# Performance work log

Measured on AMD Instinct MI355X. Metric: run time of the kernel, lower is better.

The kernel has to match this reference:

```python
import jax, jax.numpy as jnp
import numpy as np

ALPHA = 6.0
BETA = 1.8
D = 256
P = 4096


def setup_inputs() -> dict:
    key = jax.random.key(0)
    k1, k2, k3 = jax.random.split(key, 3)
    pts = jax.random.normal(k1, (1, 16384, 3), dtype=jnp.float32)
    # strict_standard_normal is a shuffled Gaussian quantile grid; a standard
    # normal draw is statistically equivalent for a correctness baseline.
    A = jax.random.normal(k2, (3, D), dtype=jnp.float32) * ALPHA
    B = jax.random.normal(k3, (3, P), dtype=jnp.float32) * BETA
    return {"pts": pts, "A": A, "B": B}


def reference(pts, A, B):
    d = A.shape[-1]
    sqrt_d = jnp.asarray(d, jnp.float32) ** 0.5
    pA = pts @ A            # (b, n, d)
    pB = pts @ B            # (b, n, p)
    eA = jnp.concatenate([jnp.cos(pA), jnp.sin(pA)], axis=-1)  # (b, n, 2d)
    eB = jnp.concatenate([jnp.cos(pB), jnp.sin(pB)], axis=-1)  # (b, n, 2p)
    # linear-attention-style chain: eB @ (eB^T @ eA)
    T = jnp.einsum('bnp,bnd->bpd', eB, eA)   # (b, 2p, 2d)
    G = jnp.einsum('bnp,bpd->bnd', eB, T)    # (b, n, 2d)
    Gc = jax.lax.complex(G[..., :d], G[..., d:]) / jax.lax.complex(eA[..., :d], eA[..., d:])
    Gc = Gc / jnp.linalg.norm(Gc, axis=-1, keepdims=True) * sqrt_d
    return Gc
```

## Files before the change

### kernel.cpp

```cpp
#include <hip/hip_runtime.h>

#define NPTS 16384
#define DH 256
#define PH 4096
#define D2 512

typedef _Float16 f16;
typedef _Float16 f16x4 __attribute__((ext_vector_type(4)));
typedef _Float16 f16x8 __attribute__((ext_vector_type(8)));
typedef float f32x4 __attribute__((ext_vector_type(4)));

__device__ f16   g_eAtS[(size_t)D2 * NPTS];
__device__ f16   g_Tt[4][D2][2*PH];
__device__ f16   g_TsS[(size_t)D2 * 2*PH];
__device__ float g_G[2][NPTS][D2];

__device__ __forceinline__ void gload16(const void* g, void* l) {
    __builtin_amdgcn_global_load_lds((const __attribute__((address_space(1))) void*)g,
                                     (__attribute__((address_space(3))) void*)l, 16, 0, 0);
}

__device__ __forceinline__ void fsincos(float x, float* s, float* c) {
    *s = __sinf(x); *c = __cosf(x);
}

__global__ __launch_bounds__(256) void ker_pre(const float* __restrict__ pts,
                                               const float* __restrict__ A) {
    const int dd = blockIdx.x;
    const int t  = threadIdx.x;
    const float a0 = A[dd], a1 = A[DH + dd], a2 = A[2*DH + dd];
    f16* rowc = &g_eAtS[(size_t)dd*NPTS + t*64];
    f16* rows = &g_eAtS[(size_t)(DH + dd)*NPTS + t*64];
    const int sx = dd & 7;
    #pragma unroll
    for (int s = 0; s < 8; ++s) {
        const int nb = t*64 + 8*(s ^ sx);
        f16x8 vc, vs;
        #pragma unroll
        for (int i = 0; i < 8; ++i) {
            const float* pr = pts + (size_t)(nb + i)*3;
            float sn, cs_; fsincos(pr[0]*a0 + pr[1]*a1 + pr[2]*a2, &sn, &cs_);
            vc[i] = (f16)cs_; vs[i] = (f16)sn;
        }
        *(f16x8*)(rowc + 8*s) = vc;
        *(f16x8*)(rows + 8*s) = vs;
    }
}

__global__ __launch_bounds__(512) void ker_T(const float* __restrict__ pts,
                                             const float* __restrict__ B) {
    const int q0 = blockIdx.x * 64;
    const int d0 = blockIdx.y * 256;
    const int ks = blockIdx.z;
    const int t  = threadIdx.x;
    const int lane = t & 63, wid = t >> 6;
    const int wm = wid >> 2, wn = wid & 3;
    const int l7 = lane & 7;

    __shared__ f16 Al[128][64];
    __shared__ f16 Bl[256][64];

    f32x4 acc[4][4];
    #pragma unroll
    for (int a = 0; a < 4; ++a)
        #pragma unroll
        for (int bq = 0; bq < 4; ++bq) acc[a][bq] = (f32x4){0.f,0.f,0.f,0.f};

    const int qq  = t >> 3;
    const int nn0 = (t & 7) * 8;
    const int wsl = ((t & 7) ^ (qq & 7)) * 8;
    const float b0 = B[q0+qq], b1 = B[PH+q0+qq], b2 = B[2*PH+q0+qq];
    const size_t bsrc0 = (size_t)(d0 + 32*wid + (lane >> 3))*NPTS + 8*l7;
    const int mrow = wm*64 + (lane & 15);
    const int ncol = wn*64 + (lane & 15);

    f16x8 vcR, vsR;

#define TSB(nb_)                                                               \
    _Pragma("unroll")                                                          \
    for (int i = 0; i < 4; ++i)                                                \
        gload16(&g_eAtS[0] + bsrc0 + (size_t)(8*i)*NPTS + (size_t)(nb_),       \
                &Bl[32*wid + 8*i][0])

#define TCOMP(nb_) do {                                                        \
    const float* pb = pts + (size_t)((nb_) + nn0)*3;                           \
    const float4 F0 = *(const float4*)(pb);                                    \
    const float4 F1 = *(const float4*)(pb + 4);                                \
    const float4 F2 = *(const float4*)(pb + 8);                                \
    const float4 F3 = *(const float4*)(pb + 12);                               \
    const float4 F4 = *(const float4*)(pb + 16);                               \
    const float4 F5 = *(const float4*)(pb + 20);                               \
    const float xx[8] = {F0.x, F0.w, F1.z, F2.y, F3.x, F3.w, F4.z, F5.y};      \
    const float yy[8] = {F0.y, F1.x, F1.w, F2.z, F3.y, F4.x, F4.w, F5.z};      \
    const float zz[8] = {F0.z, F1.y, F2.x, F2.w, F3.z, F4.y, F5.x, F5.w};      \
    _Pragma("unroll")                                                          \
    for (int u = 0; u < 8; ++u) {                                              \
        float sn, cc; fsincos(xx[u]*b0 + yy[u]*b1 + zz[u]*b2, &sn, &cc);       \
        vcR[u] = (f16)cc; vsR[u] = (f16)sn;                                    \
    }                                                                          \
} while (0)

    TCOMP(ks*4096);

    for (int c = 0; c < 64; ++c) {
        const int nb = ks*4096 + c*64;
        TSB(nb);
        *(f16x8*)&Al[qq][wsl]      = vcR;
        *(f16x8*)&Al[64 + qq][wsl] = vsR;
        __syncthreads();
        f16x8 af[2][4], bf[2][4];
        #pragma unroll
        for (int kk = 0; kk < 2; ++kk) {
            #pragma unroll
            for (int mf = 0; mf < 4; ++mf)
                af[kk][mf] = *(const f16x8*)&Al[mrow + mf*16][(((lane >> 4) + 4*kk) ^ l7)*8];
            #pragma unroll
            for (int nf = 0; nf < 4; ++nf)
                bf[kk][nf] = *(const f16x8*)&Bl[ncol + nf*16][(((lane >> 4) + 4*kk) ^ l7)*8];
        }
        if (c < 63) TCOMP(nb + 64);
        #pragma unroll
        for (int kk = 0; kk < 2; ++kk)
            #pragma unroll
            for (int mf = 0; mf < 4; ++mf)
                #pragma unroll
                for (int nf = 0; nf < 4; ++nf)
                    acc[mf][nf] = __builtin_amdgcn_mfma_f32_16x16x32_f16(
                        af[kk][mf], bf[kk][nf], acc[mf][nf], 0, 0, 0);
        asm volatile("" : "+v"(vcR), "+v"(vsR));
        __syncthreads();
    }
#undef TSB
#undef TCOMP

    #pragma unroll
    for (int mf = 0; mf < 4; ++mf) {
        const int qrow = q0 + mf*16 + (lane >> 4)*4;
        #pragma unroll
        for (int nf = 0; nf < 4; ++nf) {
            const int d = d0 + wn*64 + nf*16 + (lane & 15);
            f16x4 v;
            #pragma unroll
            for (int j = 0; j < 4; ++j) v[j] = (f16)acc[mf][nf][j];
            *(f16x4*)&g_Tt[ks][d][(size_t)wm*PH + qrow] = v;
        }
    }
}

__global__ __launch_bounds__(256) void ker_tsum() {
    const int u  = blockIdx.x*256 + threadIdx.x;
    const int d  = u >> 10;
    const int jj = u & 1023;
    const int c = jj >> 3, s = jj & 7;
    const int klb = 64*c + 8*(s ^ (d & 7));
    const int q0_ = klb >> 1;
    float oc[4] = {0,0,0,0}, os[4] = {0,0,0,0};
    #pragma unroll
    for (int z = 0; z < 4; ++z) {
        const f16x4 a  = *(const f16x4*)&g_Tt[z][d][q0_];
        const f16x4 bs = *(const f16x4*)&g_Tt[z][d][PH + q0_];
        #pragma unroll
        for (int j = 0; j < 4; ++j) { oc[j] += (float)a[j]; os[j] += (float)bs[j]; }
    }
    f16x8 v;
    #pragma unroll
    for (int j = 0; j < 4; ++j) { v[2*j] = (f16)oc[j]; v[2*j+1] = (f16)os[j]; }
    *(f16x8*)&g_TsS[(size_t)d*(2*PH) + 64*c + 8*s] = v;
}

__global__ __launch_bounds__(512) void ker_G(const float* __restrict__ pts,
                                             const float* __restrict__ B) {
    const int n0 = blockIdx.x * 128;
    const int d0 = blockIdx.y * 256;
    const int ks = blockIdx.z;
    const int t  = threadIdx.x;
    const int lane = t & 63, wid = t >> 6;
    const int wm = wid >> 2, wn = wid & 3;
    const int l7 = lane & 7;

    __shared__ f16 Al[128][64];
    __shared__ f16 Bl[256][64];

    f32x4 acc[4][4];
    #pragma unroll
    for (int a = 0; a < 4; ++a)
        #pragma unroll
        for (int bq = 0; bq < 4; ++bq) acc[a][bq] = (f32x4){0.f,0.f,0.f,0.f};

    const int nn   = t >> 2;
    const int qch8 = (t & 3) * 8;
    const int sl0  = 2*(t & 3);
    const int sx   = nn & 7;
    const float px = pts[(size_t)(n0+nn)*3];
    const float py = pts[(size_t)(n0+nn)*3 + 1];
    const float pz = pts[(size_t)(n0+nn)*3 + 2];
    const size_t bsrc0 = (size_t)(d0 + 32*wid + (lane >> 3))*(2*PH) + 8*l7;
    const int mrow = wm*64 + (lane & 15);
    const int ncol = wn*64 + (lane & 15);

    f16x8 v0R, v1R;

#define GSB(ikb_)                                                              \
    _Pragma("unroll")                                                          \
    for (int i = 0; i < 4; ++i)                                                \
        gload16(&g_TsS[0] + bsrc0 + (size_t)(8*i)*(2*PH) + (size_t)(ikb_),     \
                &Bl[32*wid + 8*i][0])

#define GCOMP(ikb_) do {                                                       \
    const int qg = ((ikb_) >> 1) + qch8;                                       \
    const float4 X0 = *(const float4*)&B[qg];                                  \
    const float4 X1 = *(const float4*)&B[qg + 4];                              \
    const float4 Y0 = *(const float4*)&B[PH + qg];                             \
    const float4 Y1 = *(const float4*)&B[PH + qg + 4];                         \
    const float4 Z0 = *(const float4*)&B[2*PH + qg];                           \
    const float4 Z1 = *(const float4*)&B[2*PH + qg + 4];                       \
    const float bx[8] = {X0.x,X0.y,X0.z,X0.w, X1.x,X1.y,X1.z,X1.w};            \
    const float by[8] = {Y0.x,Y0.y,Y0.z,Y0.w, Y1.x,Y1.y,Y1.z,Y1.w};            \
    const float bz[8] = {Z0.x,Z0.y,Z0.z,Z0.w, Z1.x,Z1.y,Z1.z,Z1.w};            \
    _Pragma("unroll")                                                          \
    for (int u = 0; u < 8; ++u) {                                              \
        float sn, cc; fsincos(px*bx[u] + py*by[u] + pz*bz[u], &sn, &cc);       \
        if (u < 4) { v0R[2*u]     = (f16)cc; v0R[2*u+1]     = (f16)sn; }       \
        else       { v1R[2*(u-4)] = (f16)cc; v1R[2*(u-4)+1] = (f16)sn; }       \
    }                                                                          \
} while (0)

    GCOMP(ks*4096);

    for (int c = 0; c < 64; ++c) {
        const int ikb = ks*4096 + c*64;
        GSB(ikb);
        *(f16x8*)&Al[nn][((sl0    ) ^ sx)*8] = v0R;
        *(f16x8*)&Al[nn][((sl0 + 1) ^ sx)*8] = v1R;
        __syncthreads();
        f16x8 af[2][4], bf[2][4];
        #pragma unroll
        for (int kk = 0; kk < 2; ++kk) {
            #pragma unroll
            for (int mf = 0; mf < 4; ++mf)
                af[kk][mf] = *(const f16x8*)&Al[mrow + mf*16][(((lane >> 4) + 4*kk) ^ l7)*8];
            #pragma unroll
            for (int nf = 0; nf < 4; ++nf)
                bf[kk][nf] = *(const f16x8*)&Bl[ncol + nf*16][(((lane >> 4) + 4*kk) ^ l7)*8];
        }
        if (c < 63) GCOMP(ikb + 64);
        #pragma unroll
        for (int kk = 0; kk < 2; ++kk)
            #pragma unroll
            for (int mf = 0; mf < 4; ++mf)
                #pragma unroll
                for (int nf = 0; nf < 4; ++nf)
                    acc[mf][nf] = __builtin_amdgcn_mfma_f32_16x16x32_f16(
                        af[kk][mf], bf[kk][nf], acc[mf][nf], 0, 0, 0);
        asm volatile("" : "+v"(v0R), "+v"(v1R));
        __syncthreads();
    }
#undef GSB
#undef GCOMP

    #pragma unroll
    for (int mf = 0; mf < 4; ++mf) {
        const int nbase = n0 + wm*64 + mf*16 + (lane >> 4)*4;
        #pragma unroll
        for (int nf = 0; nf < 4; ++nf) {
            const int d = d0 + wn*64 + nf*16 + (lane & 15);
            #pragma unroll
            for (int j = 0; j < 4; ++j)
                g_G[ks][nbase + j][d] = acc[mf][nf][j];
        }
    }
}

__global__ __launch_bounds__(256) void ker_fin(const float* __restrict__ pts,
                                               const float* __restrict__ A,
                                               float* __restrict__ out) {
    const int n = blockIdx.x;
    const int k = threadIdx.x;
    const float p0 = pts[(size_t)n*3], p1 = pts[(size_t)n*3+1], p2 = pts[(size_t)n*3+2];
    const float alp = p0*A[k] + p1*A[DH + k] + p2*A[2*DH + k];
    float sa, ca; fsincos(alp, &sa, &ca);
    const float Gr = g_G[0][n][k]      + g_G[1][n][k];
    const float Gi = g_G[0][n][DH + k] + g_G[1][n][DH + k];
    const float Re = Gr*ca + Gi*sa;
    float nr = Gr*Gr + Gi*Gi;
    #pragma unroll
    for (int off = 32; off > 0; off >>= 1) nr += __shfl_down(nr, off, 64);
    __shared__ float wsum[4];
    if ((k & 63) == 0) wsum[k >> 6] = nr;
    __syncthreads();
    const float total = wsum[0] + wsum[1] + wsum[2] + wsum[3];
    const float scale = 16.0f * rsqrtf(total);
    out[(size_t)n*DH + k] = Re * scale;
}

extern "C" void kernel_launch(void* const* d_in, const int* in_sizes, int n_in,
                              void* d_out, int out_size, void* d_ws, size_t ws_size,
                              hipStream_t stream) {
    const float* pts = (const float*)d_in[0];
    const float* A   = (const float*)d_in[1];
    const float* B   = (const float*)d_in[2];
    float* out = (float*)d_out;
    (void)d_ws; (void)ws_size; (void)out_size;

    ker_pre <<<256, 256, 0, stream>>>(pts, A);
    ker_T   <<<dim3(64, 2, 4), 512, 0, stream>>>(pts, B);
    ker_tsum<<<2048, 256, 0, stream>>>();
    ker_G   <<<dim3(128, 2, 2), 512, 0, stream>>>(pts, B);
    ker_fin <<<16384, 256, 0, stream>>>(pts, A, out);
}
```

Before: 363.1 us.

## Pipeline GEMM k-loop with triple-buffered async B loads and double-buffered A tile

Both GEMM kernels (T and G) move from a 64-wide k step with one shared buffer and two full syncthreads per step to a 32-wide k step. The B tile is triple-buffered and fetched asynchronously two steps ahead with direct global-to-LDS loads. The A tile is double-buffered and written by the on-the-fly sin/cos computation, with a single barrier per step guarded by explicit vmcnt/lgkmcnt waits. Global intermediate layouts lose their XOR swizzle, and LDS bank conflicts are instead avoided with a padded A row stride and a lane-dependent rotation on B reads. The goal is to overlap memory latency with MFMA work and halve barriers per k element, at the cost of twice as many loop iterations and hand-tuned wait counts that could be fragile.

```diff
diff --git a/kernel.cpp b/kernel.cpp
--- a/kernel.cpp
+++ b/kernel.cpp
@@ -4,15 +4,16 @@
 #define DH 256
 #define PH 4096
 #define D2 512
+#define LDA 40
 
 typedef _Float16 f16;
 typedef _Float16 f16x4 __attribute__((ext_vector_type(4)));
 typedef _Float16 f16x8 __attribute__((ext_vector_type(8)));
 typedef float f32x4 __attribute__((ext_vector_type(4)));
 
-__device__ f16   g_eAtS[(size_t)D2 * NPTS];
+__device__ f16   g_eAt[D2][NPTS];
 __device__ f16   g_Tt[4][D2][2*PH];
-__device__ f16   g_TsS[(size_t)D2 * 2*PH];
+__device__ f16   g_Ts[D2][2*PH];
 __device__ float g_G[2][NPTS][D2];
 
 __device__ __forceinline__ void gload16(const void* g, void* l) {
@@ -29,12 +30,11 @@
     const int dd = blockIdx.x;
     const int t  = threadIdx.x;
     const float a0 = A[dd], a1 = A[DH + dd], a2 = A[2*DH + dd];
-    f16* rowc = &g_eAtS[(size_t)dd*NPTS + t*64];
-    f16* rows = &g_eAtS[(size_t)(DH + dd)*NPTS + t*64];
-    const int sx = dd & 7;
+    f16* rowc = &g_eAt[dd][t*64];
+    f16* rows = &g_eAt[DH + dd][t*64];
     #pragma unroll
     for (int s = 0; s < 8; ++s) {
-        const int nb = t*64 + 8*(s ^ sx);
+        const int nb = t*64 + 8*s;
         f16x8 vc, vs;
         #pragma unroll
         for (int i = 0; i < 8; ++i) {
@@ -55,10 +55,9 @@
     const int t  = threadIdx.x;
     const int lane = t & 63, wid = t >> 6;
     const int wm = wid >> 2, wn = wid & 3;
-    const int l7 = lane & 7;
-
-    __shared__ f16 Al[128][64];
-    __shared__ f16 Bl[256][64];
+
+    __shared__ f16 Al[2][128][LDA];
+    __shared__ f16 Bl[3][256][32];
 
     f32x4 acc[4][4];
     #pragma unroll
@@ -67,71 +66,75 @@
         for (int bq = 0; bq < 4; ++bq) acc[a][bq] = (f32x4){0.f,0.f,0.f,0.f};
 
     const int qq  = t >> 3;
-    const int nn0 = (t & 7) * 8;
-    const int wsl = ((t & 7) ^ (qq & 7)) * 8;
+    const int nn0 = (t & 7) * 4;
     const float b0 = B[q0+qq], b1 = B[PH+q0+qq], b2 = B[2*PH+q0+qq];
-    const size_t bsrc0 = (size_t)(d0 + 32*wid + (lane >> 3))*NPTS + 8*l7;
+    const int phiL = (((lane >> 2) & 3) + (lane >> 4)) & 3;
+    const size_t bsrc0 = (size_t)(d0 + 32*wid + (lane >> 2))*NPTS
+                       + 8 * ((lane & 3) ^ phiL);
     const int mrow = wm*64 + (lane & 15);
     const int ncol = wn*64 + (lane & 15);
-
-    f16x8 vcR, vsR;
-
-#define TSB(nb_)                                                               \
+    const int akof = (lane >> 4) * 8;
+    const int phib = ((lane & 3) + ((lane >> 2) & 3)) & 3;
+    const int bkof = ((lane >> 4) ^ phib) * 8;
+
+#define TSB(rg, nb_) do {                                                      \
+    gload16(&g_eAt[0][0] + bsrc0 + (size_t)(nb_),              &Bl[rg][32*wid][0]);      \
+    gload16(&g_eAt[0][0] + bsrc0 + (size_t)16*NPTS + (size_t)(nb_), &Bl[rg][32*wid+16][0]); \
+} while (0)
+
+#define TRIG(ab, nb_) do {                                                     \
+    const float* pb = pts + (size_t)((nb_) + nn0)*3;                           \
+    const float4 P0 = *(const float4*)(pb);                                    \
+    const float4 P1 = *(const float4*)(pb + 4);                                \
+    const float4 P2 = *(const float4*)(pb + 8);                                \
+    const float xx[4] = {P0.x, P0.w, P1.z, P2.y};                              \
+    const float yy[4] = {P0.y, P1.x, P1.w, P2.z};                              \
+    const float zz[4] = {P0.z, P1.y, P2.x, P2.w};                              \
+    f16x4 vc, vs;                                                              \
     _Pragma("unroll")                                                          \
-    for (int i = 0; i < 4; ++i)                                                \
-        gload16(&g_eAtS[0] + bsrc0 + (size_t)(8*i)*NPTS + (size_t)(nb_),       \
-                &Bl[32*wid + 8*i][0])
-
-#define TCOMP(nb_) do {                                                        \
-    const float* pb = pts + (size_t)((nb_) + nn0)*3;                           \
-    const float4 F0 = *(const float4*)(pb);                                    \
-    const float4 F1 = *(const float4*)(pb + 4);                                \
-    const float4 F2 = *(const float4*)(pb + 8);                                \
-    const float4 F3 = *(const float4*)(pb + 12);                               \
-    const float4 F4 = *(const float4*)(pb + 16);                               \
-    const float4 F5 = *(const float4*)(pb + 20);                               \
-    const float xx[8] = {F0.x, F0.w, F1.z, F2.y, F3.x, F3.w, F4.z, F5.y};      \
-    const float yy[8] = {F0.y, F1.x, F1.w, F2.z, F3.y, F4.x, F4.w, F5.z};      \
-    const float zz[8] = {F0.z, F1.y, F2.x, F2.w, F3.z, F4.y, F5.x, F5.w};      \
-    _Pragma("unroll")                                                          \
-    for (int u = 0; u < 8; ++u) {                                              \
+    for (int u = 0; u < 4; ++u) {                                              \
         float sn, cc; fsincos(xx[u]*b0 + yy[u]*b1 + zz[u]*b2, &sn, &cc);       \
-        vcR[u] = (f16)cc; vsR[u] = (f16)sn;                                    \
+        vc[u] = (f16)cc; vs[u] = (f16)sn;                                      \
     }                                                                          \
+    *(f16x4*)&Al[ab][qq][nn0]      = vc;                                       \
+    *(f16x4*)&Al[ab][64 + qq][nn0] = vs;                                       \
 } while (0)
 
-    TCOMP(ks*4096);
-
-    for (int c = 0; c < 64; ++c) {
-        const int nb = ks*4096 + c*64;
-        TSB(nb);
-        *(f16x8*)&Al[qq][wsl]      = vcR;
-        *(f16x8*)&Al[64 + qq][wsl] = vsR;
-        __syncthreads();
-        f16x8 af[2][4], bf[2][4];
-        #pragma unroll
-        for (int kk = 0; kk < 2; ++kk) {
-            #pragma unroll
-            for (int mf = 0; mf < 4; ++mf)
-                af[kk][mf] = *(const f16x8*)&Al[mrow + mf*16][(((lane >> 4) + 4*kk) ^ l7)*8];
+    const int base = ks*4096;
+    TRIG(0, base);
+    TSB(0, base); TSB(1, base + 32);
+    asm volatile("s_waitcnt vmcnt(2)" ::: "memory");
+    asm volatile("s_waitcnt lgkmcnt(0)" ::: "memory");
+    __builtin_amdgcn_s_barrier();
+    __builtin_amdgcn_sched_barrier(0);
+
+    int bcur = 0, bprf = 2;
+    for (int c = 0; c < 128; ++c) {
+        const int nb = base + c*32;
+        if (c < 127) TRIG((c + 1) & 1, nb + 32);
+        f16x8 af[4], bf[4];
+        #pragma unroll
+        for (int mf = 0; mf < 4; ++mf)
+            af[mf] = *(const f16x8*)&Al[c & 1][mrow + mf*16][akof];
+        #pragma unroll
+        for (int nf = 0; nf < 4; ++nf)
+            bf[nf] = *(const f16x8*)&Bl[bcur][ncol + nf*16][bkof];
+        #pragma unroll
+        for (int mf = 0; mf < 4; ++mf)
             #pragma unroll
             for (int nf = 0; nf < 4; ++nf)
-                bf[kk][nf] = *(const f16x8*)&Bl[ncol + nf*16][(((lane >> 4) + 4*kk) ^ l7)*8];
-        }
-        if (c < 63) TCOMP(nb + 64);
-        #pragma unroll
-        for (int kk = 0; kk < 2; ++kk)
-            #pragma unroll
-            for (int mf = 0; mf < 4; ++mf)
-                #pragma unroll
-                for (int nf = 0; nf < 4; ++nf)
-                    acc[mf][nf] = __builtin_amdgcn_mfma_f32_16x16x32_f16(
-                        af[kk][mf], bf[kk][nf], acc[mf][nf], 0, 0, 0);
-        asm volatile("" : "+v"(vcR), "+v"(vsR));
-        __syncthreads();
+                acc[mf][nf] = __builtin_amdgcn_mfma_f32_16x16x32_f16(
+                    af[mf], bf[nf], acc[mf][nf], 0, 0, 0);
+        if (c < 126) TSB(bprf, nb + 64);
+        asm volatile("s_waitcnt vmcnt(2)" ::: "memory");
+        asm volatile("s_waitcnt lgkmcnt(0)" ::: "memory");
+        __builtin_amdgcn_s_barrier();
+        __builtin_amdgcn_sched_barrier(0);
+        bcur = (bcur == 2) ? 0 : bcur + 1;
+        bprf = (bprf == 2) ? 0 : bprf + 1;
     }
 #undef TSB
-#undef TCOMP
+#undef TRIG
 
     #pragma unroll
     for (int mf = 0; mf < 4; ++mf) {
@@ -151,9 +154,7 @@
     const int u  = blockIdx.x*256 + threadIdx.x;
     const int d  = u >> 10;
     const int jj = u & 1023;
-    const int c = jj >> 3, s = jj & 7;
-    const int klb = 64*c + 8*(s ^ (d & 7));
-    const int q0_ = klb >> 1;
+    const int q0_ = jj * 4;
     float oc[4] = {0,0,0,0}, os[4] = {0,0,0,0};
     #pragma unroll
     for (int z = 0; z < 4; ++z) {
@@ -165,7 +166,7 @@
     f16x8 v;
     #pragma unroll
     for (int j = 0; j < 4; ++j) { v[2*j] = (f16)oc[j]; v[2*j+1] = (f16)os[j]; }
-    *(f16x8*)&g_TsS[(size_t)d*(2*PH) + 64*c + 8*s] = v;
+    *(f16x8*)&g_Ts[d][jj*8] = v;
 }
 
 __global__ __launch_bounds__(512) void ker_G(const float* __restrict__ pts,
@@ -176,10 +177,9 @@
     const int t  = threadIdx.x;
     const int lane = t & 63, wid = t >> 6;
     const int wm = wid >> 2, wn = wid & 3;
-    const int l7 = lane & 7;
-
-    __shared__ f16 Al[128][64];
-    __shared__ f16 Bl[256][64];
+
+    __shared__ f16 Al[2][128][LDA];
+    __shared__ f16 Bl[3][256][32];
 
     f32x4 acc[4][4];
     #pragma unroll
@@ -187,76 +187,78 @@
         #pragma unroll
         for (int bq = 0; bq < 4; ++bq) acc[a][bq] = (f32x4){0.f,0.f,0.f,0.f};
 
-    const int nn   = t >> 2;
-    const int qch8 = (t & 3) * 8;
-    const int sl0  = 2*(t & 3);
-    const int sx   = nn & 7;
+    const int nn  = t >> 2;
+    const int ikc = (t & 3) * 8;
+    const int qc4 = (t & 3) * 4;
     const float px = pts[(size_t)(n0+nn)*3];
     const float py = pts[(size_t)(n0+nn)*3 + 1];
     const float pz = pts[(size_t)(n0+nn)*3 + 2];
-    const size_t bsrc0 = (size_t)(d0 + 32*wid + (lane >> 3))*(2*PH) + 8*l7;
+    const int phiL = (((lane >> 2) & 3) + (lane >> 4)) & 3;
+    const size_t bsrc0 = (size_t)(d0 + 32*wid + (lane >> 2))*(2*PH)
+                       + 8 * ((lane & 3) ^ phiL);
     const int mrow = wm*64 + (lane & 15);
     const int ncol = wn*64 + (lane & 15);
-
-    f16x8 v0R, v1R;
-
-#define GSB(ikb_)                                                              \
+    const int akof = (lane >> 4) * 8;
+    const int phib = ((lane & 3) + ((lane >> 2) & 3)) & 3;
+    const int bkof = ((lane >> 4) ^ phib) * 8;
+
+#define GSB(rg, ikb_) do {                                                     \
+    gload16(&g_Ts[0][0] + bsrc0 + (size_t)(ikb_),                 &Bl[rg][32*wid][0]);      \
+    gload16(&g_Ts[0][0] + bsrc0 + (size_t)16*(2*PH) + (size_t)(ikb_), &Bl[rg][32*wid+16][0]); \
+} while (0)
+
+#define GTRIG(ab, ikb_) do {                                                   \
+    const int qg = ((ikb_) >> 1) + qc4;                                        \
+    const float4 X0 = *(const float4*)&B[qg];                                  \
+    const float4 Y0 = *(const float4*)&B[PH + qg];                             \
+    const float4 Z0 = *(const float4*)&B[2*PH + qg];                           \
+    const float bx[4] = {X0.x, X0.y, X0.z, X0.w};                              \
+    const float by[4] = {Y0.x, Y0.y, Y0.z, Y0.w};                              \
+    const float bz[4] = {Z0.x, Z0.y, Z0.z, Z0.w};                              \
+    f16x8 vv;                                                                  \
     _Pragma("unroll")                                                          \
-    for (int i = 0; i < 4; ++i)                                                \
-        gload16(&g_TsS[0] + bsrc0 + (size_t)(8*i)*(2*PH) + (size_t)(ikb_),     \
-                &Bl[32*wid + 8*i][0])
-
-#define GCOMP(ikb_) do {                                                       \
-    const int qg = ((ikb_) >> 1) + qch8;                                       \
-    const float4 X0 = *(const float4*)&B[qg];                                  \
-    const float4 X1 = *(const float4*)&B[qg + 4];                              \
-    const float4 Y0 = *(const float4*)&B[PH + qg];                             \
-    const float4 Y1 = *(const float4*)&B[PH + qg + 4];                         \
-    const float4 Z0 = *(const float4*)&B[2*PH + qg];                           \
-    const float4 Z1 = *(const float4*)&B[2*PH + qg + 4];                       \
-    const float bx[8] = {X0.x,X0.y,X0.z,X0.w, X1.x,X1.y,X1.z,X1.w};            \
-    const float by[8] = {Y0.x,Y0.y,Y0.z,Y0.w, Y1.x,Y1.y,Y1.z,Y1.w};            \
-    const float bz[8] = {Z0.x,Z0.y,Z0.z,Z0.w, Z1.x,Z1.y,Z1.z,Z1.w};            \
-    _Pragma("unroll")                                                          \
-    for (int u = 0; u < 8; ++u) {                                              \
+    for (int u = 0; u < 4; ++u) {                                              \
         float sn, cc; fsincos(px*bx[u] + py*by[u] + pz*bz[u], &sn, &cc);       \
-        if (u < 4) { v0R[2*u]     = (f16)cc; v0R[2*u+1]     = (f16)sn; }       \
-        else       { v1R[2*(u-4)] = (f16)cc; v1R[2*(u-4)+1] = (f16)sn; }       \
+        vv[2*u] = (f16)cc; vv[2*u+1] = (f16)sn;                                \
     }                                                                          \
+    *(f16x8*)&Al[ab][nn][ikc] = vv;                                            \
 } while (0)
 
-    GCOMP(ks*4096);
-
-    for (int c = 0; c < 64; ++c) {
-        const int ikb = ks*4096 + c*64;
-        GSB(ikb);
-        *(f16x8*)&Al[nn][((sl0    ) ^ sx)*8] = v0R;
-        *(f16x8*)&Al[nn][((sl0 + 1) ^ sx)*8] = v1R;
-        __syncthreads();
-        f16x8 af[2][4], bf[2][4];
-        #pragma unroll
-        for (int kk = 0; kk < 2; ++kk) {
-            #pragma unroll
-            for (int mf = 0; mf < 4; ++mf)
-                af[kk][mf] = *(const f16x8*)&Al[mrow + mf*16][(((lane >> 4) + 4*kk) ^ l7)*8];
+    const int base = ks*4096;
+    GTRIG(0, base);
+    GSB(0, base); GSB(1, base + 32);
+    asm volatile("s_waitcnt vmcnt(2)" ::: "memory");
+    asm volatile("s_waitcnt lgkmcnt(0)" ::: "memory");
+    __builtin_amdgcn_s_barrier();
+    __builtin_amdgcn_sched_barrier(0);
+
+    int bcur = 0, bprf = 2;
+    for (int c = 0; c < 128; ++c) {
+        const int ikb = base + c*32;
+        if (c < 127) GTRIG((c + 1) & 1, ikb + 32);
+        f16x8 af[4], bf[4];
+        #pragma unroll
+        for (int mf = 0; mf < 4; ++mf)
+            af[mf] = *(const f16x8*)&Al[c & 1][mrow + mf*16][akof];
+        #pragma unroll
+        for (int nf = 0; nf < 4; ++nf)
+            bf[nf] = *(const f16x8*)&Bl[bcur][ncol + nf*16][bkof];
+        #pragma unroll
+        for (int mf = 0; mf < 4; ++mf)
             #pragma unroll
             for (int nf = 0; nf < 4; ++nf)
-                bf[kk][nf] = *(const f16x8*)&Bl[ncol + nf*16][(((lane >> 4) + 4*kk) ^ l7)*8];
-        }
-        if (c < 63) GCOMP(ikb + 64);
-        #pragma unroll
-        for (int kk = 0; kk < 2; ++kk)
-            #pragma unroll
-            for (int mf = 0; mf < 4; ++mf)
-                #pragma unroll
-                for (int nf = 0; nf < 4; ++nf)
-                    acc[mf][nf] = __builtin_amdgcn_mfma_f32_16x16x32_f16(
-                        af[kk][mf], bf[kk][nf], acc[mf][nf], 0, 0, 0);
-        asm volatile("" : "+v"(v0R), "+v"(v1R));
-        __syncthreads();
+                acc[mf][nf] = __builtin_amdgcn_mfma_f32_16x16x32_f16(
+                    af[mf], bf[nf], acc[mf][nf], 0, 0, 0);
+        if (c < 126) GSB(bprf, ikb + 64);
+        asm volatile("s_waitcnt vmcnt(2)" ::: "memory");
+        asm volatile("s_waitcnt lgkmcnt(0)" ::: "memory");
+        __builtin_amdgcn_s_barrier();
+        __builtin_amdgcn_sched_barrier(0);
+        bcur = (bcur == 2) ? 0 : bcur + 1;
+        bprf = (bprf == 2) ? 0 : bprf + 1;
     }
 #undef GSB
-#undef GCOMP
+#undef GTRIG
 
     #pragma unroll
     for (int mf = 0; mf < 4; ++mf) {
```

New measurement: 398.5 us. 9.8% more time.
